# Optimization experiments

Measured on AMD Instinct MI355X. Metric: run time of the kernel, lower is better.

The kernel has to match this reference:

```python
import jax, jax.numpy as jnp
import numpy as np

N_LAYERS = 512
Z_INI = 0.0
DEL_Z = 0.9 / 512.0
MU = 1.0
BATCH = 131072


def setup_inputs() -> dict:
    key = jax.random.key(0)
    k1, k2, k3, k4 = jax.random.split(key, 4)
    Re_s = 0.1 * jax.random.normal(k1, (BATCH,), dtype=jnp.float32)
    Im_s = 0.1 * jax.random.normal(k2, (BATCH,), dtype=jnp.float32)
    # omega kept away from 0 (appears in a denominator)
    omega = jax.random.uniform(k3, (BATCH,), dtype=jnp.float32, minval=0.5, maxval=1.5)
    PiT = jnp.ones((1,), dtype=jnp.float32)
    # Bs[j] is Linear(1,1,bias=False)(ones) == its scalar weight; keep near 1 for stability
    B = 1.0 + 0.02 * jax.random.normal(k4, (N_LAYERS + 1,), dtype=jnp.float32)
    return {"Re_s": Re_s, "Im_s": Im_s, "omega": omega, "PiT": PiT, "B": B}


def reference(Re_s, Im_s, omega, PiT, B):
    # forward_1: Euler integration, strict sequential dependence -> lax.scan
    zs = Z_INI + DEL_Z * jnp.arange(N_LAYERS, dtype=jnp.float32)
    B1s = B[:-1]  # Bs[j]
    B2s = B[1:]   # Bs[j+1]
    mu2 = MU * MU

    def step(carry, x):
        Re, Im = carry
        b1, b2, z = x
        inv1 = 1.0 / (PiT * (1.0 - z))          # 1/(PiT (1-z))
        inv2 = inv1 / (1.0 - z)                  # 1/(PiT (1-z)^2)
        g = 1.0 - b2 / b1
        # NOTE: torch updates Re first; Im update uses the NEW Re
        Re_n = Re + g * (Re + inv1) + DEL_Z * (
            2.0 * omega * Im * Re + 2.0 * omega * Im * inv1 - inv2
        )
        Im_n = Im + g * Im + DEL_Z * (
            -omega * inv2 / PiT
            - 2.0 * omega * inv1 * Re_n
            + omega * Im * Im
            - omega * Re_n * Re_n
            + omega / (b1 * b1)
            - z * z * mu2 / (b1 * omega)
        )
        return (Re_n, Im_n), None

    (Re_f, Im_f), _ = jax.lax.scan(step, (Re_s, Im_s), (B1s, B2s, zs))
    return (Re_f, Im_f)
```

## Files before the change

kernel.cpp:

```cpp
#include <hip/hip_runtime.h>

#define N_LAYERS 512
#define DEL_Z (0.9f / 512.0f)

__global__ __launch_bounds__(256) void metric_scan_kernel(
    const float* __restrict__ Re_s, const float* __restrict__ Im_s,
    const float* __restrict__ omega, const float* __restrict__ PiT_p,
    const float* __restrict__ B, float* __restrict__ out, int n)
{
    __shared__ float4 cA[N_LAYERS];
    __shared__ float  cB[N_LAYERS];

    const float PiT = PiT_p[0];
    for (int l = threadIdx.x; l < N_LAYERS; l += 256) {
        const float z    = DEL_Z * (float)l;
        const float b1   = B[l];
        const float b2   = B[l + 1];
        const float omz  = 1.0f - z;
        const float inv1 = 1.0f / (PiT * omz);
        const float inv2 = inv1 / omz;
        const float g    = 1.0f - b2 / b1;
        const float c0   = 1.0f + g;
        const float c1   = g * inv1 - DEL_Z * inv2;
        const float c3   = inv1 * inv1 - inv2 / PiT + 1.0f / (b1 * b1);
        const float c4   = DEL_Z * z * z / b1;
        cA[l] = make_float4(c0, c1, inv1, c3);
        cB[l] = c4;
    }
    __syncthreads();

    const int i = blockIdx.x * 256 + threadIdx.x;
    float Re = Re_s[i];
    float Im = Im_s[i];
    const float om    = omega[i];
    const float dzom  = DEL_Z * om;
    const float dz2om = 2.0f * dzom;
    const float iom   = 1.0f / om;

    #pragma unroll 8
    for (int l = 0; l < N_LAYERS; ++l) {
        const float4 c  = cA[l];
        const float  c4 = cB[l];
        const float  t  = Re + c.z;
        const float  a  = fmaf(c.x, Re, c.y);
        const float  Rn = fmaf(dz2om * Im, t, a);
        const float  u  = Rn + c.z;
        float s = fmaf(Im, Im, c.w);
        s = fmaf(-u, u, s);
        const float b = fmaf(c.x, Im, -(c4 * iom));
        Im = fmaf(dzom, s, b);
        Re = Rn;
    }

    out[i]     = Re;
    out[n + i] = Im;
}

extern "C" void kernel_launch(void* const* d_in, const int* in_sizes, int n_in,
                              void* d_out, int out_size, void* d_ws, size_t ws_size,
                              hipStream_t stream)
{
    const float* Re_s  = (const float*)d_in[0];
    const float* Im_s  = (const float*)d_in[1];
    const float* omega = (const float*)d_in[2];
    const float* PiT   = (const float*)d_in[3];
    const float* B     = (const float*)d_in[4];
    float* out = (float*)d_out;
    const int n = in_sizes[0];
    metric_scan_kernel<<<n / 256, 256, 0, stream>>>(Re_s, Im_s, omega, PiT, B, out, n);
}
```

Measured before the change: 21.57 us.

## Reformulate recurrence in shifted variable with compile-time layer constants and full unroll

Rewrites the per-step update in terms of T = PiT*Re + 1/(1-z), so that z-dependent terms become compile-time constants embedded as immediates via constexpr helpers. The shared-memory table shrinks to two floats per layer, loaded as float4 with software prefetch, and the 512-step loop is fully unrolled. This is meant to cut the dependent-instruction count and LDS traffic per step. In exchange the code grows considerably, the shift assumes a fixed final offset (T - 10) tied to DEL_Z*512 = 0.9, and it could change float rounding behaviour.

Result: slower. 67.59 us (+213.4%).

```diff
diff --git a/kernel.cpp b/kernel.cpp
--- a/kernel.cpp
+++ b/kernel.cpp
@@ -2,57 +2,80 @@
 
 #define N_LAYERS 512
 #define DEL_Z (0.9f / 512.0f)
+
+constexpr double DZD = 0.9 / 512.0;
+__host__ __device__ constexpr float K1f(int l) {
+    double k = 1.0 / (1.0 - DZD * (double)l);
+    return (float)(-DZD * k * k);
+}
+__host__ __device__ constexpr float K2f(int l) {
+    double k  = 1.0 / (1.0 - DZD * (double)l);
+    double kn = 1.0 / (1.0 - DZD * (double)(l + 1));
+    return (float)(kn - k);
+}
+__host__ __device__ constexpr float K3f(int l) {
+    double z = DZD * (double)l;
+    return (float)(DZD * z * z);
+}
+
+#define STEP(C0, R1, L)                                         \
+    {                                                           \
+        const float e  = fmaf(dz2om, Im, (C0));                 \
+        const float U  = fmaf(e, T, K1f(L));                    \
+        const float u  = U * ip;                                \
+        const float pk = K3f(L) * phi;                          \
+        const float w  = (R1) + pk;                             \
+        const float cw = (R1) * w;                              \
+        float s = fmaf(Im, Im, cw);                             \
+        s = fmaf(-u, u, s);                                     \
+        const float bm = (C0) * Im;                             \
+        Im = fmaf(dzom, s, bm);                                 \
+        T  = U + K2f(L);                                        \
+    }
 
 __global__ __launch_bounds__(256) void metric_scan_kernel(
     const float* __restrict__ Re_s, const float* __restrict__ Im_s,
     const float* __restrict__ omega, const float* __restrict__ PiT_p,
     const float* __restrict__ B, float* __restrict__ out, int n)
 {
-    __shared__ float4 cA[N_LAYERS];
-    __shared__ float  cB[N_LAYERS];
+    __shared__ float2 cg[N_LAYERS];
 
-    const float PiT = PiT_p[0];
     for (int l = threadIdx.x; l < N_LAYERS; l += 256) {
-        const float z    = DEL_Z * (float)l;
-        const float b1   = B[l];
-        const float b2   = B[l + 1];
-        const float omz  = 1.0f - z;
-        const float inv1 = 1.0f / (PiT * omz);
-        const float inv2 = inv1 / omz;
-        const float g    = 1.0f - b2 / b1;
-        const float c0   = 1.0f + g;
-        const float c1   = g * inv1 - DEL_Z * inv2;
-        const float c3   = inv1 * inv1 - inv2 / PiT + 1.0f / (b1 * b1);
-        const float c4   = DEL_Z * z * z / b1;
-        cA[l] = make_float4(c0, c1, inv1, c3);
-        cB[l] = c4;
+        const float b1 = B[l];
+        const float b2 = B[l + 1];
+        cg[l] = make_float2(2.0f - b2 / b1, 1.0f / b1);
     }
     __syncthreads();
 
     const int i = blockIdx.x * 256 + threadIdx.x;
-    float Re = Re_s[i];
     float Im = Im_s[i];
-    const float om    = omega[i];
-    const float dzom  = DEL_Z * om;
+    const float om   = omega[i];
+    const float PiT  = PiT_p[0];
+    const float ip   = 1.0f / PiT;
+    const float dzom = DEL_Z * om;
     const float dz2om = 2.0f * dzom;
-    const float iom   = 1.0f / om;
+    const float iom  = 1.0f / om;
+    const float phi  = -(iom * iom) * (512.0f / 0.9f);
+    float T = fmaf(PiT, Re_s[i], 1.0f);
 
-    #pragma unroll 8
-    for (int l = 0; l < N_LAYERS; ++l) {
-        const float4 c  = cA[l];
-        const float  c4 = cB[l];
-        const float  t  = Re + c.z;
-        const float  a  = fmaf(c.x, Re, c.y);
-        const float  Rn = fmaf(dz2om * Im, t, a);
-        const float  u  = Rn + c.z;
-        float s = fmaf(Im, Im, c.w);
-        s = fmaf(-u, u, s);
-        const float b = fmaf(c.x, Im, -(c4 * iom));
-        Im = fmaf(dzom, s, b);
-        Re = Rn;
+    const float4* cf4 = (const float4*)cg;
+    float4 bA = cf4[0];
+    float4 bB = cf4[1];
+
+    #pragma unroll
+    for (int g = 0; g < N_LAYERS / 4; ++g) {
+        const int j2 = (2 * g + 2 < N_LAYERS / 2) ? 2 * g + 2 : N_LAYERS / 2 - 1;
+        const int j3 = (2 * g + 3 < N_LAYERS / 2) ? 2 * g + 3 : N_LAYERS / 2 - 1;
+        const float4 nA = cf4[j2];
+        const float4 nB = cf4[j3];
+        STEP(bA.x, bA.y, 4 * g + 0)
+        STEP(bA.z, bA.w, 4 * g + 1)
+        STEP(bB.x, bB.y, 4 * g + 2)
+        STEP(bB.z, bB.w, 4 * g + 3)
+        bA = nA; bB = nB;
     }
 
-    out[i]     = Re;
+    out[i]     = (T - 10.0f) * ip;
     out[n + i] = Im;
 }
 
```
